# Kernel tuning notes

Measured on AMD Instinct MI355X. Metric: run time of the kernel, lower is better.

Reference implementation:

```python
import jax, jax.numpy as jnp
import numpy as np

B, S, D = 64, 4096, 256

def setup_inputs() -> dict:
    key = jax.random.key(0)
    k1, k2, k3 = jax.random.split(key, 3)
    x = jax.random.normal(k1, (B, S, D), dtype=jnp.float32)
    # glorot-scale params
    W = jax.random.normal(k2, (D, D), dtype=jnp.float32) * (1.0 / np.sqrt(D))
    b = jnp.zeros((D,), dtype=jnp.float32)
    u = jax.random.normal(k3, (D, 1), dtype=jnp.float32) * (1.0 / np.sqrt(D))
    return {"x": x, "W": W, "b": b, "u": u}

def reference(x, W, b, u):
    # uit: [B,S,D] = tanh(x @ W + b)
    uit = jnp.tanh(jnp.einsum('bsd,de->bse', x, W) + b)
    # score: [B,S]
    score = jnp.einsum('bsd,d->bs', uit, u[:, 0])
    weights = jax.nn.softmax(score, axis=1)          # [B,S]
    context = jnp.einsum('bs,bsd->bd', weights, x)   # [B,D]
    return (context, weights)
```

## Files before the change

kernel.cpp:

```cpp
#include <hip/hip_runtime.h>
#include <hip/hip_bf16.h>
#include <cstdint>
#include <cstddef>

#define B_ 64
#define S_ 4096
#define D_ 256
#define BM 64
#define BK 32
#define NBLK (B_ * S_ / BM)
#define BLKS_PER_B (S_ / BM)

typedef __attribute__((ext_vector_type(8))) short short8;
typedef __attribute__((ext_vector_type(4))) float f32x4;
typedef __attribute__((ext_vector_type(4))) float f4;

__device__ __forceinline__ short f2bf(float f) {
  union { float f; uint32_t u; } v; v.f = f;
  uint32_t r = v.u + 0x7FFFu + ((v.u >> 16) & 1u);
  return (short)(r >> 16);
}

__device__ __forceinline__ float fast_tanh(float z) {
  return 1.0f - 2.0f * __builtin_amdgcn_rcpf(__expf(2.0f * z) + 1.0f);
}

__device__ __forceinline__ void gload_lds16(const short* g, short* l) {
  __builtin_amdgcn_global_load_lds(
      (const __attribute__((address_space(1))) int*)(g),
      (__attribute__((address_space(3))) int*)(l), 16, 0, 0);
}

__global__ void k_pack(const float* __restrict__ W, short* __restrict__ wt) {
  __shared__ float tile[64][65];
  int t = blockIdx.x, ti = t >> 2, tj = t & 3;
  int tid = threadIdx.x;
#pragma unroll
  for (int i = 0; i < 4; ++i) {
    int idx = i * 1024 + tid;
    int r = idx >> 6, c = idx & 63;
    tile[c][r] = W[(ti * 64 + r) * 256 + tj * 64 + c];
  }
  __syncthreads();
#pragma unroll
  for (int i = 0; i < 4; ++i) {
    int idx = i * 1024 + tid;
    int r = idx >> 6, c = idx & 63;
    wt[(tj * 64 + r) * 256 + ti * 64 + c] = f2bf(tile[r][c]);
  }
}

#define WAITV(N) asm volatile("s_waitcnt vmcnt(" #N ")" ::: "memory")
#define FENCE()  asm volatile("" ::: "memory")

#define STAGE(BUF, KC)                                                        \
  {                                                                           \
    _Pragma("unroll")                                                         \
    for (int i_ = 0; i_ < 4; ++i_) {                                          \
      int c_ = i_ * 256 + tid;                                                \
      int n_ = c_ >> 2, ko_ = (c_ & 3) * 8;                                   \
      gload_lds16(wt + n_ * 256 + (KC) * 32 + ko_, &lsB[BUF][c_ * 8]);        \
    }                                                                         \
  }

#define ITER(KC, VM, SCA, SCB, SLA, SLB, DOSTAGE, DOLOAD)                     \
  {                                                                           \
    if (DOSTAGE) STAGE(((KC) + 1) & 1, (KC) + 1);                             \
    if (DOLOAD) {                                                             \
      SLA = *(const f4*)(xrow + ((KC) + 2) * 32);                             \
      SLB = *(const f4*)(xrow + ((KC) + 2) * 32 + 4);                         \
    }                                                                         \
    WAITV(VM);                                                                \
    asm volatile("s_waitcnt lgkmcnt(0)" ::: "memory");                        \
    __builtin_amdgcn_sched_barrier(0);                                        \
    __builtin_amdgcn_s_barrier();                                             \
    FENCE();                                                                  \
    short8 fr_;                                                               \
    fr_[0]=f2bf(SCA[0]); fr_[1]=f2bf(SCA[1]); fr_[2]=f2bf(SCA[2]); fr_[3]=f2bf(SCA[3]); \
    fr_[4]=f2bf(SCB[0]); fr_[5]=f2bf(SCB[1]); fr_[6]=f2bf(SCB[2]); fr_[7]=f2bf(SCB[3]); \
    _Pragma("unroll")                                                         \
    for (int nf_ = 0; nf_ < 16; ++nf_) {                                      \
      short8 bfr_ = *(const short8*)&lsB[(KC) & 1][(nf_ * 16 + cl) * 32 + gr * 8]; \
      acc[nf_] = __builtin_amdgcn_mfma_f32_16x16x32_bf16(fr_, bfr_, acc[nf_], 0, 0, 0); \
    }                                                                         \
    FENCE();                                                                  \
    __builtin_amdgcn_s_barrier();                                             \
    FENCE();                                                                  \
  }

__global__ __launch_bounds__(256, 3)
void k_scores(const float* __restrict__ x, const short* __restrict__ wt,
              const float* __restrict__ bias, const float* __restrict__ u,
              float* __restrict__ ws_scores, float* __restrict__ ws_m,
              float* __restrict__ ws_l, float* __restrict__ ws_c) {
  __shared__ __align__(16) short lsB[2][D_ * BK];
  __shared__ __align__(8) float bu[D_ * 2];
  __shared__ float score_lds[BM];
  __shared__ float e_lds[BM];
  __shared__ float red_lds[1];

  const int tid  = threadIdx.x;
  const int bid  = blockIdx.x;
  const int m0   = bid * BM;
  const int lane = tid & 63;
  const int wv   = tid >> 6;
  const int cl   = lane & 15;
  const int gr   = lane >> 4;

  bu[tid * 2]     = bias[tid];
  bu[tid * 2 + 1] = u[tid];

  f32x4 acc[16];
#pragma unroll
  for (int j = 0; j < 16; ++j) acc[j] = (f32x4){0.f, 0.f, 0.f, 0.f};

  const float* xrow = x + (size_t)(m0 + wv * 16 + cl) * D_ + gr * 8;

  f4 s0a, s0b, s1a, s1b, s2a, s2b;
  s0a = *(const f4*)(xrow);       s0b = *(const f4*)(xrow + 4);
  STAGE(0, 0);
  s1a = *(const f4*)(xrow + 32);  s1b = *(const f4*)(xrow + 36);

  ITER(0, 8, s0a, s0b, s2a, s2b, 1, 1)
  ITER(1, 8, s1a, s1b, s0a, s0b, 1, 1)
  ITER(2, 8, s2a, s2b, s1a, s1b, 1, 1)
  ITER(3, 8, s0a, s0b, s2a, s2b, 1, 1)
  ITER(4, 8, s1a, s1b, s0a, s0b, 1, 1)
  ITER(5, 8, s2a, s2b, s1a, s1b, 1, 1)
  ITER(6, 6, s0a, s0b, s0a, s0b, 1, 0)
  ITER(7, 0, s1a, s1b, s0a, s0b, 0, 0)

  float p0 = 0.f, p1 = 0.f, p2 = 0.f, p3 = 0.f;
#pragma unroll
  for (int nf = 0; nf < 16; ++nf) {
    float bb = bu[(nf * 16 + cl) * 2];
    float uu = bu[(nf * 16 + cl) * 2 + 1];
    p0 += fast_tanh(acc[nf][0] + bb) * uu;
    p1 += fast_tanh(acc[nf][1] + bb) * uu;
    p2 += fast_tanh(acc[nf][2] + bb) * uu;
    p3 += fast_tanh(acc[nf][3] + bb) * uu;
  }
#pragma unroll
  for (int m = 1; m < 16; m <<= 1) {
    p0 += __shfl_xor(p0, m);
    p1 += __shfl_xor(p1, m);
    p2 += __shfl_xor(p2, m);
    p3 += __shfl_xor(p3, m);
  }
  if (cl == 0) {
    int r = wv * 16 + gr * 4;
    score_lds[r + 0] = p0;
    score_lds[r + 1] = p1;
    score_lds[r + 2] = p2;
    score_lds[r + 3] = p3;
    ws_scores[m0 + r + 0] = p0;
    ws_scores[m0 + r + 1] = p1;
    ws_scores[m0 + r + 2] = p2;
    ws_scores[m0 + r + 3] = p3;
  }
  __syncthreads();
  if (tid < 64) {
    float v = score_lds[tid];
#pragma unroll
    for (int m = 32; m >= 1; m >>= 1) v = fmaxf(v, __shfl_xor(v, m));
    if (tid == 0) red_lds[0] = v;
  }
  __syncthreads();
  float mb = red_lds[0];
  if (tid < BM) e_lds[tid] = __expf(score_lds[tid] - mb);
  __syncthreads();
  if (tid < 64) {
    float v = e_lds[tid];
#pragma unroll
    for (int m = 32; m >= 1; m >>= 1) v += __shfl_xor(v, m);
    if (tid == 0) { ws_m[bid] = mb; ws_l[bid] = v; }
  }
  float cacc = 0.f;
  const float* xp = x + (size_t)m0 * D_ + tid;
#pragma unroll 4
  for (int s = 0; s < BM; ++s) cacc += e_lds[s] * xp[(size_t)s * D_];
  ws_c[bid * D_ + tid] = cacc;
}

__global__ void k_combine(const float* __restrict__ ws_m, const float* __restrict__ ws_l,
                          const float* __restrict__ ws_c, float* __restrict__ out_ctx,
                          float* __restrict__ ws_M, float* __restrict__ ws_L) {
  int b = blockIdx.x, d = threadIdx.x;
  float M = -3.4e38f;
#pragma unroll
  for (int i = 0; i < BLKS_PER_B; ++i) M = fmaxf(M, ws_m[b * BLKS_PER_B + i]);
  float L = 0.f, c = 0.f;
#pragma unroll 4
  for (int i = 0; i < BLKS_PER_B; ++i) {
    float f = __expf(ws_m[b * BLKS_PER_B + i] - M);
    L += ws_l[b * BLKS_PER_B + i] * f;
    c += ws_c[(size_t)(b * BLKS_PER_B + i) * D_ + d] * f;
  }
  out_ctx[b * D_ + d] = c / L;
  if (d == 0) { ws_M[b] = M; ws_L[b] = L; }
}

__global__ void k_weights(const float* __restrict__ ws_scores, const float* __restrict__ ws_M,
                          const float* __restrict__ ws_L, float* __restrict__ out_w) {
  int idx = blockIdx.x * 256 + threadIdx.x;
  int b = idx >> 12;
  out_w[idx] = __expf(ws_scores[idx] - ws_M[b]) / ws_L[b];
}

extern "C" void kernel_launch(void* const* d_in, const int* in_sizes, int n_in,
                              void* d_out, int out_size, void* d_ws, size_t ws_size,
                              hipStream_t stream) {
  (void)in_sizes; (void)n_in; (void)out_size; (void)ws_size;
  const float* x    = (const float*)d_in[0];
  const float* W    = (const float*)d_in[1];
  const float* bias = (const float*)d_in[2];
  const float* u    = (const float*)d_in[3];
  float* out_ctx = (float*)d_out;
  float* out_w   = (float*)d_out + B_ * D_;

  char* ws = (char*)d_ws;
  short* wt        = (short*)(ws + 0);
  float* ws_scores = (float*)(ws + 131072);
  float* ws_m      = (float*)(ws + 1179648);
  float* ws_l      = (float*)(ws + 1196032);
  float* ws_c      = (float*)(ws + 1212416);
  float* ws_M      = (float*)(ws + 5406720);
  float* ws_L      = (float*)(ws + 5406976);

  hipLaunchKernelGGL(k_pack, dim3(16), dim3(1024), 0, stream, W, wt);
  hipLaunchKernelGGL(k_scores, dim3(NBLK), dim3(256), 0, stream,
                     x, wt, bias, u, ws_scores, ws_m, ws_l, ws_c);
  hipLaunchKernelGGL(k_combine, dim3(B_), dim3(256), 0, stream,
                     ws_m, ws_l, ws_c, out_ctx, ws_M, ws_L);
  hipLaunchKernelGGL(k_weights, dim3(B_ * S_ / 256), dim3(256), 0, stream,
                     ws_scores, ws_M, ws_L, out_w);
}
```

Before: 115.9 us.

## Hold W fragments in registers and stage bf16 x tile in swizzled LDS

Rewrites the score kernel so that each wave keeps a 64-column slice of packed W in registers, replacing double-buffered LDS staging of W. The full 64x256 x tile is converted to bf16 once and written into XOR-swizzled LDS, and all MFMAs then run without per-k barriers. Per-wave partial scores are reduced across waves through LDS, and the max and sum reductions are merged into one pass. The cost is high register pressure from 32 short8 B fragments, which lowers launch bounds occupancy from 3 to 2 and loses overlap between loading x and doing the math.

```diff
diff --git a/kernel.cpp b/kernel.cpp
--- a/kernel.cpp
+++ b/kernel.cpp
@@ -7,7 +7,6 @@
 #define S_ 4096
 #define D_ 256
 #define BM 64
-#define BK 32
 #define NBLK (B_ * S_ / BM)
 #define BLKS_PER_B (S_ / BM)
 
@@ -25,12 +24,6 @@
   return 1.0f - 2.0f * __builtin_amdgcn_rcpf(__expf(2.0f * z) + 1.0f);
 }
 
-__device__ __forceinline__ void gload_lds16(const short* g, short* l) {
-  __builtin_amdgcn_global_load_lds(
-      (const __attribute__((address_space(1))) int*)(g),
-      (__attribute__((address_space(3))) int*)(l), 16, 0, 0);
-}
-
 __global__ void k_pack(const float* __restrict__ W, short* __restrict__ wt) {
   __shared__ float tile[64][65];
   int t = blockIdx.x, ti = t >> 2, tj = t & 3;
@@ -50,52 +43,13 @@
   }
 }
 
-#define WAITV(N) asm volatile("s_waitcnt vmcnt(" #N ")" ::: "memory")
-#define FENCE()  asm volatile("" ::: "memory")
-
-#define STAGE(BUF, KC)                                                        \
-  {                                                                           \
-    _Pragma("unroll")                                                         \
-    for (int i_ = 0; i_ < 4; ++i_) {                                          \
-      int c_ = i_ * 256 + tid;                                                \
-      int n_ = c_ >> 2, ko_ = (c_ & 3) * 8;                                   \
-      gload_lds16(wt + n_ * 256 + (KC) * 32 + ko_, &lsB[BUF][c_ * 8]);        \
-    }                                                                         \
-  }
-
-#define ITER(KC, VM, SCA, SCB, SLA, SLB, DOSTAGE, DOLOAD)                     \
-  {                                                                           \
-    if (DOSTAGE) STAGE(((KC) + 1) & 1, (KC) + 1);                             \
-    if (DOLOAD) {                                                             \
-      SLA = *(const f4*)(xrow + ((KC) + 2) * 32);                             \
-      SLB = *(const f4*)(xrow + ((KC) + 2) * 32 + 4);                         \
-    }                                                                         \
-    WAITV(VM);                                                                \
-    asm volatile("s_waitcnt lgkmcnt(0)" ::: "memory");                        \
-    __builtin_amdgcn_sched_barrier(0);                                        \
-    __builtin_amdgcn_s_barrier();                                             \
-    FENCE();                                                                  \
-    short8 fr_;                                                               \
-    fr_[0]=f2bf(SCA[0]); fr_[1]=f2bf(SCA[1]); fr_[2]=f2bf(SCA[2]); fr_[3]=f2bf(SCA[3]); \
-    fr_[4]=f2bf(SCB[0]); fr_[5]=f2bf(SCB[1]); fr_[6]=f2bf(SCB[2]); fr_[7]=f2bf(SCB[3]); \
-    _Pragma("unroll")                                                         \
-    for (int nf_ = 0; nf_ < 16; ++nf_) {                                      \
-      short8 bfr_ = *(const short8*)&lsB[(KC) & 1][(nf_ * 16 + cl) * 32 + gr * 8]; \
-      acc[nf_] = __builtin_amdgcn_mfma_f32_16x16x32_bf16(fr_, bfr_, acc[nf_], 0, 0, 0); \
-    }                                                                         \
-    FENCE();                                                                  \
-    __builtin_amdgcn_s_barrier();                                             \
-    FENCE();                                                                  \
-  }
-
-__global__ __launch_bounds__(256, 3)
+__global__ __launch_bounds__(256, 2)
 void k_scores(const float* __restrict__ x, const short* __restrict__ wt,
               const float* __restrict__ bias, const float* __restrict__ u,
               float* __restrict__ ws_scores, float* __restrict__ ws_m,
               float* __restrict__ ws_l, float* __restrict__ ws_c) {
-  __shared__ __align__(16) short lsB[2][D_ * BK];
-  __shared__ __align__(8) float bu[D_ * 2];
-  __shared__ float score_lds[BM];
+  __shared__ __align__(16) short lsA[BM * D_];
+  __shared__ float score_part[BM][4];
   __shared__ float e_lds[BM];
   __shared__ float red_lds[1];
 
@@ -107,78 +61,115 @@
   const int cl   = lane & 15;
   const int gr   = lane >> 4;
 
-  bu[tid * 2]     = bias[tid];
-  bu[tid * 2 + 1] = u[tid];
-
-  f32x4 acc[16];
-#pragma unroll
-  for (int j = 0; j < 16; ++j) acc[j] = (f32x4){0.f, 0.f, 0.f, 0.f};
-
-  const float* xrow = x + (size_t)(m0 + wv * 16 + cl) * D_ + gr * 8;
-
-  f4 s0a, s0b, s1a, s1b, s2a, s2b;
-  s0a = *(const f4*)(xrow);       s0b = *(const f4*)(xrow + 4);
-  STAGE(0, 0);
-  s1a = *(const f4*)(xrow + 32);  s1b = *(const f4*)(xrow + 36);
-
-  ITER(0, 8, s0a, s0b, s2a, s2b, 1, 1)
-  ITER(1, 8, s1a, s1b, s0a, s0b, 1, 1)
-  ITER(2, 8, s2a, s2b, s1a, s1b, 1, 1)
-  ITER(3, 8, s0a, s0b, s2a, s2b, 1, 1)
-  ITER(4, 8, s1a, s1b, s0a, s0b, 1, 1)
-  ITER(5, 8, s2a, s2b, s1a, s1b, 1, 1)
-  ITER(6, 6, s0a, s0b, s0a, s0b, 1, 0)
-  ITER(7, 0, s1a, s1b, s0a, s0b, 0, 0)
-
-  float p0 = 0.f, p1 = 0.f, p2 = 0.f, p3 = 0.f;
-#pragma unroll
-  for (int nf = 0; nf < 16; ++nf) {
-    float bb = bu[(nf * 16 + cl) * 2];
-    float uu = bu[(nf * 16 + cl) * 2 + 1];
-    p0 += fast_tanh(acc[nf][0] + bb) * uu;
-    p1 += fast_tanh(acc[nf][1] + bb) * uu;
-    p2 += fast_tanh(acc[nf][2] + bb) * uu;
-    p3 += fast_tanh(acc[nf][3] + bb) * uu;
-  }
-#pragma unroll
-  for (int m = 1; m < 16; m <<= 1) {
-    p0 += __shfl_xor(p0, m);
-    p1 += __shfl_xor(p1, m);
-    p2 += __shfl_xor(p2, m);
-    p3 += __shfl_xor(p3, m);
-  }
-  if (cl == 0) {
-    int r = wv * 16 + gr * 4;
-    score_lds[r + 0] = p0;
-    score_lds[r + 1] = p1;
-    score_lds[r + 2] = p2;
-    score_lds[r + 3] = p3;
-    ws_scores[m0 + r + 0] = p0;
-    ws_scores[m0 + r + 1] = p1;
-    ws_scores[m0 + r + 2] = p2;
-    ws_scores[m0 + r + 3] = p3;
-  }
-  __syncthreads();
+  short8 b0[8], b1[8], b2[8], b3[8];
+  {
+    const short* wb = wt + (wv * 64 + cl) * 256 + gr * 8;
+#pragma unroll
+    for (int kf = 0; kf < 8; ++kf) {
+      b0[kf] = *(const short8*)(wb + kf * 32);
+      b1[kf] = *(const short8*)(wb + 16 * 256 + kf * 32);
+      b2[kf] = *(const short8*)(wb + 32 * 256 + kf * 32);
+      b3[kf] = *(const short8*)(wb + 48 * 256 + kf * 32);
+    }
+  }
+  const float bb0 = bias[wv * 64 + cl],      uu0 = u[wv * 64 + cl];
+  const float bb1 = bias[wv * 64 + 16 + cl], uu1 = u[wv * 64 + 16 + cl];
+  const float bb2 = bias[wv * 64 + 32 + cl], uu2 = u[wv * 64 + 32 + cl];
+  const float bb3 = bias[wv * 64 + 48 + cl], uu3 = u[wv * 64 + 48 + cl];
+
+  {
+    const int srow = tid >> 2;
+    const int scol = (tid & 3) * 64;
+    const float* xs = x + (size_t)(m0 + srow) * D_ + scol;
+    char* wbase = (char*)lsA + srow * 512;
+    const int sxor = (srow & 7) << 4;
+#pragma unroll
+    for (int i = 0; i < 8; ++i) {
+      f4 g0 = *(const f4*)(xs + i * 8);
+      f4 g1 = *(const f4*)(xs + i * 8 + 4);
+      short8 s;
+      s[0]=f2bf(g0[0]); s[1]=f2bf(g0[1]); s[2]=f2bf(g0[2]); s[3]=f2bf(g0[3]);
+      s[4]=f2bf(g1[0]); s[5]=f2bf(g1[1]); s[6]=f2bf(g1[2]); s[7]=f2bf(g1[3]);
+      *(short8*)(wbase + ((scol * 2 + i * 16) ^ sxor)) = s;
+    }
+  }
+  __syncthreads();
+
+  f32x4 acc[4][4];
+#pragma unroll
+  for (int i = 0; i < 4; ++i)
+#pragma unroll
+    for (int j = 0; j < 4; ++j)
+      acc[i][j] = (f32x4){0.f, 0.f, 0.f, 0.f};
+
+  const int axor = (cl & 7) << 4;
+#pragma unroll
+  for (int rfp = 0; rfp < 4; rfp += 2) {
+    const char* ar0 = (const char*)lsA + (rfp * 16 + cl) * 512;
+    const char* ar1 = ar0 + 16 * 512;
+#pragma unroll
+    for (int kf = 0; kf < 8; ++kf) {
+      const int ko = (kf * 64 + gr * 16) ^ axor;
+      short8 a0 = *(const short8*)(ar0 + ko);
+      short8 a1 = *(const short8*)(ar1 + ko);
+      acc[rfp][0]     = __builtin_amdgcn_mfma_f32_16x16x32_bf16(a0, b0[kf], acc[rfp][0], 0, 0, 0);
+      acc[rfp][1]     = __builtin_amdgcn_mfma_f32_16x16x32_bf16(a0, b1[kf], acc[rfp][1], 0, 0, 0);
+      acc[rfp][2]     = __builtin_amdgcn_mfma_f32_16x16x32_bf16(a0, b2[kf], acc[rfp][2], 0, 0, 0);
+      acc[rfp][3]     = __builtin_amdgcn_mfma_f32_16x16x32_bf16(a0, b3[kf], acc[rfp][3], 0, 0, 0);
+      acc[rfp + 1][0] = __builtin_amdgcn_mfma_f32_16x16x32_bf16(a1, b0[kf], acc[rfp + 1][0], 0, 0, 0);
+      acc[rfp + 1][1] = __builtin_amdgcn_mfma_f32_16x16x32_bf16(a1, b1[kf], acc[rfp + 1][1], 0, 0, 0);
+      acc[rfp + 1][2] = __builtin_amdgcn_mfma_f32_16x16x32_bf16(a1, b2[kf], acc[rfp + 1][2], 0, 0, 0);
+      acc[rfp + 1][3] = __builtin_amdgcn_mfma_f32_16x16x32_bf16(a1, b3[kf], acc[rfp + 1][3], 0, 0, 0);
+    }
+  }
+
+#pragma unroll
+  for (int rf = 0; rf < 4; ++rf) {
+    float p0 = fast_tanh(acc[rf][0][0] + bb0) * uu0 + fast_tanh(acc[rf][1][0] + bb1) * uu1
+             + fast_tanh(acc[rf][2][0] + bb2) * uu2 + fast_tanh(acc[rf][3][0] + bb3) * uu3;
+    float p1 = fast_tanh(acc[rf][0][1] + bb0) * uu0 + fast_tanh(acc[rf][1][1] + bb1) * uu1
+             + fast_tanh(acc[rf][2][1] + bb2) * uu2 + fast_tanh(acc[rf][3][1] + bb3) * uu3;
+    float p2 = fast_tanh(acc[rf][0][2] + bb0) * uu0 + fast_tanh(acc[rf][1][2] + bb1) * uu1
+             + fast_tanh(acc[rf][2][2] + bb2) * uu2 + fast_tanh(acc[rf][3][2] + bb3) * uu3;
+    float p3 = fast_tanh(acc[rf][0][3] + bb0) * uu0 + fast_tanh(acc[rf][1][3] + bb1) * uu1
+             + fast_tanh(acc[rf][2][3] + bb2) * uu2 + fast_tanh(acc[rf][3][3] + bb3) * uu3;
+#pragma unroll
+    for (int m = 1; m < 16; m <<= 1) {
+      p0 += __shfl_xor(p0, m);
+      p1 += __shfl_xor(p1, m);
+      p2 += __shfl_xor(p2, m);
+      p3 += __shfl_xor(p3, m);
+    }
+    if (cl == 0) {
+      int r = rf * 16 + gr * 4;
+      score_part[r + 0][wv] = p0;
+      score_part[r + 1][wv] = p1;
+      score_part[r + 2][wv] = p2;
+      score_part[r + 3][wv] = p3;
+    }
+  }
+  __syncthreads();
+
   if (tid < 64) {
-    float v = score_lds[tid];
-#pragma unroll
-    for (int m = 32; m >= 1; m >>= 1) v = fmaxf(v, __shfl_xor(v, m));
-    if (tid == 0) red_lds[0] = v;
-  }
-  __syncthreads();
-  float mb = red_lds[0];
-  if (tid < BM) e_lds[tid] = __expf(score_lds[tid] - mb);
-  __syncthreads();
-  if (tid < 64) {
-    float v = e_lds[tid];
-#pragma unroll
-    for (int m = 32; m >= 1; m >>= 1) v += __shfl_xor(v, m);
-    if (tid == 0) { ws_m[bid] = mb; ws_l[bid] = v; }
-  }
+    float s = score_part[tid][0] + score_part[tid][1] +
+              score_part[tid][2] + score_part[tid][3];
+    float mx = s;
+#pragma unroll
+    for (int m = 32; m >= 1; m >>= 1) mx = fmaxf(mx, __shfl_xor(mx, m));
+    float e = __expf(s - mx);
+    e_lds[tid] = e;
+    float l = e;
+#pragma unroll
+    for (int m = 32; m >= 1; m >>= 1) l += __shfl_xor(l, m);
+    ws_scores[m0 + tid] = s;
+    if (tid == 0) { ws_m[bid] = mx; ws_l[bid] = l; red_lds[0] = mx; }
+  }
+  __syncthreads();
+
   float cacc = 0.f;
   const float* xp = x + (size_t)m0 * D_ + tid;
 #pragma unroll 4
-  for (int s = 0; s < BM; ++s) cacc += e_lds[s] * xp[(size_t)s * D_];
+  for (int s = 0; s < BM; ++s) cacc = fmaf(e_lds[s], xp[(size_t)s * D_], cacc);
   ws_c[bid * D_ + tid] = cacc;
 }
 
```

Result: slower. 165.9 us (+43.1%).
